# Kernel tuning notes

Measured on AMD Instinct MI355X. Metric: run time of the kernel, lower is better.

Reference implementation:

```python
import jax, jax.numpy as jnp
import numpy as np

N, D, H, O, E, K = 16384, 512, 512, 64, 8, 2


def _layernorm(x, g, b, eps=1e-5):
    mu = jnp.mean(x, axis=-1, keepdims=True)
    var = jnp.var(x, axis=-1, keepdims=True)
    return (x - mu) * jax.lax.rsqrt(var + eps) * g + b


def _gelu(x):
    return jax.nn.gelu(x, approximate=False)  # torch nn.GELU default (erf)


def setup_inputs() -> dict:
    key = jax.random.key(0)
    ks = jax.random.split(key, 20)
    s = 0.02
    return {
        "x": jax.random.normal(ks[0], (N, D), jnp.float32),
        # gate: Linear(D,H) -> LN(H) -> GELU -> Linear(H,E)
        "g_w1": jax.random.normal(ks[1], (D, H), jnp.float32) * s,
        "g_b1": jnp.zeros((H,), jnp.float32),
        "g_ln_g": jnp.ones((H,), jnp.float32),
        "g_ln_b": jnp.zeros((H,), jnp.float32),
        "g_w2": jax.random.normal(ks[2], (H, E), jnp.float32) * s,
        "g_b2": jnp.zeros((E,), jnp.float32),
        # experts (stacked over E): Linear(D,H)+LN+GELU, Linear(H,H)+LN+GELU, Linear(H,O)
        "e_w1": jax.random.normal(ks[3], (E, D, H), jnp.float32) * s,
        "e_b1": jnp.zeros((E, H), jnp.float32),
        "e_ln1_g": jnp.ones((E, H), jnp.float32),
        "e_ln1_b": jnp.zeros((E, H), jnp.float32),
        "e_w2": jax.random.normal(ks[4], (E, H, H), jnp.float32) * s,
        "e_b2": jnp.zeros((E, H), jnp.float32),
        "e_ln2_g": jnp.ones((E, H), jnp.float32),
        "e_ln2_b": jnp.zeros((E, H), jnp.float32),
        "e_w3": jax.random.normal(ks[5], (E, H, O), jnp.float32) * s,
        "e_b3": jnp.zeros((E, O), jnp.float32),
        # output projection Linear(O,O)
        "p_w": jax.random.normal(ks[6], (O, O), jnp.float32) * s,
        "p_b": jnp.zeros((O,), jnp.float32),
    }


def reference(x, g_w1, g_b1, g_ln_g, g_ln_b, g_w2, g_b2,
              e_w1, e_b1, e_ln1_g, e_ln1_b, e_w2, e_b2, e_ln2_g, e_ln2_b,
              e_w3, e_b3, p_w, p_b):
    n = x.shape[0]
    # --- gate ---
    gh = _gelu(_layernorm(x @ g_w1 + g_b1, g_ln_g, g_ln_b))
    gate_logits = gh @ g_w2 + g_b2                      # [N, E]
    gate_weights = jax.nn.softmax(gate_logits, axis=-1)
    top_k_weights, top_k_indices = jax.lax.top_k(gate_weights, K)
    top_k_weights = top_k_weights / jnp.sum(top_k_weights, axis=-1, keepdims=True)
    # dense per-token expert weights [N, E] (sum of top-k weights routed to each expert)
    w_dense = jnp.zeros((n, e_w1.shape[0]), x.dtype).at[
        jnp.arange(n)[:, None], top_k_indices].add(top_k_weights)
    # --- all experts on all tokens (faithful to dense loop) ---
    h1 = _gelu(_layernorm(jnp.einsum('nd,edh->enh', x, e_w1) + e_b1[:, None, :],
                          e_ln1_g[:, None, :], e_ln1_b[:, None, :]))
    h2 = _gelu(_layernorm(jnp.einsum('enh,ehk->enk', h1, e_w2) + e_b2[:, None, :],
                          e_ln2_g[:, None, :], e_ln2_b[:, None, :]))
    expert_out = jnp.einsum('enh,eho->eno', h2, e_w3) + e_b3[:, None, :]  # [E, N, O]
    combined = jnp.einsum('ne,eno->no', w_dense, expert_out)              # [N, O]
    output = combined @ p_w + p_b
    expert_usage = jnp.mean(gate_weights, axis=0)
    return (output, gate_weights, top_k_indices, top_k_weights, expert_usage)
```

## Files before the change

### kernel.cpp

```cpp
#include <hip/hip_runtime.h>
#include <hip/hip_bf16.h>

#define N_TOK 16384
#define MAX_SLOTS 34080
#define MAX_BLOCKS 216

typedef __attribute__((ext_vector_type(8))) short bf16x8;
typedef __attribute__((ext_vector_type(4))) float f32x4;
typedef unsigned short u16;

__device__ __forceinline__ u16 f2bf(float f) {
  __hip_bfloat16 h = __float2bfloat16(f);
  union { __hip_bfloat16 b; u16 u; } c; c.b = h; return c.u;
}
__device__ __forceinline__ float bfbits2f(u16 u) {
  return __uint_as_float(((unsigned)u) << 16);
}
__device__ __forceinline__ float gelu_erf(float x) {
  return 0.5f * x * (1.0f + erff(x * 0.70710678118654752f));
}
__device__ __forceinline__ float gelu_fast(float x) {
  float u = x * (0.79788456f + 0.035677408f * x * x);
  float ex;
  asm("v_exp_f32 %0, %1" : "=v"(ex) : "v"(-2.8853901f * u));
  float den = 1.0f + ex;
  float r;
  asm("v_rcp_f32 %0, %1" : "=v"(r) : "v"(den));
  return x * r;
}
__device__ __forceinline__ void gload16(const u16* g, char* lds) {
  __builtin_amdgcn_global_load_lds(
      (const __attribute__((address_space(1))) void*)g,
      (__attribute__((address_space(3))) void*)lds, 16, 0, 0);
}

__global__ __launch_bounds__(256) void prep_x(const float* __restrict__ x,
                                              u16* __restrict__ xbf,
                                              u16* __restrict__ xlo) {
  size_t i = (size_t)blockIdx.x * 256 + threadIdx.x;
  float4 v = ((const float4*)x)[i];
  float a[4] = {v.x, v.y, v.z, v.w};
  union { u16 us[4]; unsigned long long ll; } hb, lb;
#pragma unroll
  for (int j = 0; j < 4; ++j) {
    u16 hu = f2bf(a[j]);
    hb.us[j] = hu;
    lb.us[j] = f2bf(a[j] - bfbits2f(hu));
  }
  *(unsigned long long*)(xbf + i * 4) = hb.ll;
  *(unsigned long long*)(xlo + i * 4) = lb.ll;
}

template <int C>
__global__ __launch_bounds__(256) void pack_w(const float* __restrict__ src,
                                              u16* __restrict__ dst, int R) {
  __shared__ float tl[64][65];
  const int e = blockIdx.z;
  const int k0 = blockIdx.x * 64, n0 = blockIdx.y * 64;
  const float* s = src + (size_t)e * R * C;
  const int tr = threadIdx.x >> 2;
  const int tc4 = (threadIdx.x & 3) * 16;
#pragma unroll
  for (int j = 0; j < 4; ++j) {
    float4 v = *(const float4*)(s + (size_t)(k0 + tr) * C + n0 + tc4 + j * 4);
    tl[tr][tc4 + j * 4 + 0] = v.x;
    tl[tr][tc4 + j * 4 + 1] = v.y;
    tl[tr][tc4 + j * 4 + 2] = v.z;
    tl[tr][tc4 + j * 4 + 3] = v.w;
  }
  __syncthreads();
  const int nl = threadIdx.x >> 2;
  const int kl = (threadIdx.x & 3) * 16;
  const int n = n0 + nl;
  const int sx = (n >> 1) & 3;
  const int t = (k0 + kl) >> 5;
  const int q0 = ((k0 + kl) & 31) >> 3;
#pragma unroll
  for (int c = 0; c < 2; ++c) {
    int q = q0 + c;
    int p = q ^ sx;
    union { u16 us[8]; unsigned long long ll[2]; } o;
#pragma unroll
    for (int j = 0; j < 8; ++j) o.us[j] = f2bf(tl[kl + c * 8 + j][nl]);
    u16* d = dst + (((size_t)e * (R / 32) + t) * C + n) * 32 + p * 8;
    ((unsigned long long*)d)[0] = o.ll[0];
    ((unsigned long long*)d)[1] = o.ll[1];
  }
}

__global__ __launch_bounds__(256) void prep_wcat(const float* __restrict__ gw1,
                                                 u16* __restrict__ wp) {
  int idx = blockIdx.x * 256 + threadIdx.x;
  int p = idx & 3;
  int n = (idx >> 2) & 511;
  int t = idx >> 11;
  int q = p ^ ((n >> 1) & 3);
  int k0 = t * 32 + q * 8;
  union { u16 us[8]; unsigned long long ll[2]; } o;
#pragma unroll
  for (int j = 0; j < 8; ++j) {
    int k = k0 + j;
    u16 v;
    if (k < 512) {
      v = f2bf(gw1[k * 512 + n]);
    } else if (k < 1024) {
      float w = gw1[(k - 512) * 512 + n];
      v = f2bf(w - bfbits2f(f2bf(w)));
    } else {
      v = f2bf(gw1[(k - 1024) * 512 + n]);
    }
    o.us[j] = v;
  }
  unsigned long long* d = (unsigned long long*)(wp + (size_t)idx * 8);
  d[0] = o.ll[0];
  d[1] = o.ll[1];
}

__global__ __launch_bounds__(256) void prep_w2t(const float* __restrict__ gw2,
                                                float* __restrict__ w2t) {
  int i = blockIdx.x * 256 + threadIdx.x;
  int e = i >> 9, k = i & 511;
  w2t[i] = gw2[k * 8 + e];
}

template <int FM, int ROUTED, int GATHER, int LNOUT, int FAST>
__global__ __launch_bounds__(512, 2) void gemm_core(
    const u16* __restrict__ A, const u16* __restrict__ A2,
    const u16* __restrict__ Wp, long w_estride, int klen, long osplit,
    const float* __restrict__ bias, int b_estride,
    const float* __restrict__ lng, const float* __restrict__ lnb,
    u16* __restrict__ outb, float* __restrict__ outf,
    const int* __restrict__ slot_token, const int* __restrict__ blk_e,
    const int* __restrict__ blk_tok0) {
  constexpr int BM = FM * 32;
  constexpr int AG = FM * 2;
  constexpr int ABYTES = BM * 64;
  constexpr int BUF = ABYTES + 32768;
  constexpr int NL = AG + 32;
  constexpr int L = (NL + 7) / 8;
  constexpr int TSU = 16384;
  extern __shared__ char smem[];

  const int tid = threadIdx.x;
  const int lane = tid & 63;
  const int wv = tid >> 6;
  const int wm = (wv & 1) * (FM * 16);
  const int wn = (wv >> 1) * 128;
  const int l15 = lane & 15;
  const int lk = lane >> 4;
  const int swzk16 = (lk ^ ((l15 >> 1) & 3)) << 4;

  int e, row0, kt0, kbase;
  if (ROUTED) {
    e = blk_e[blockIdx.x];
    if (e < 0) return;
    row0 = blk_tok0[blockIdx.x];
    kt0 = 0; kbase = 0;
  } else {
    e = 0;
    row0 = blockIdx.x * BM;
    kbase = blockIdx.y * klen;
    kt0 = kbase >> 5;
  }
  const u16* We = Wp + (size_t)e * w_estride;

  const int lrq = lane >> 2;
  const int cse = (((lane & 3) ^ ((lane >> 3) & 3)) << 3);
  size_t off[L];
  int ldsoff[L], typ[L];
#pragma unroll
  for (int i = 0; i < L; ++i) {
    int id = wv + 8 * i;
    if (id >= NL) { typ[i] = 2; off[i] = 0; ldsoff[i] = 0; continue; }
    if (id < AG) {
      int lr = id * 16 + lrq;
      long grow = GATHER ? (long)slot_token[row0 + lr] : (long)(row0 + lr);
      off[i] = (size_t)grow * 512 + cse;
      ldsoff[i] = id * 1024 + lane * 16;
      typ[i] = 0;
    } else {
      int bg = id - AG;
      off[i] = (size_t)bg * 512 + lane * 8;
      ldsoff[i] = ABYTES + bg * 1024 + lane * 16;
      typ[i] = 1;
    }
  }

  auto STAGE = [&](int t, char* b) {
    const int kg = kbase + t * 32;
    const u16* Aseg = A;
    int kc = kg;
    if (A2) {
      if (kg >= 1024) { Aseg = A2; kc = kg - 1024; }
      else if (kg >= 512) kc = kg - 512;
    }
    const u16* Bt = We + (size_t)(kt0 + t) * TSU;
#pragma unroll
    for (int i = 0; i < L; ++i) {
      if (typ[i] == 0)      gload16(Aseg + off[i] + kc, b + ldsoff[i]);
      else if (typ[i] == 1) gload16(Bt + off[i], b + ldsoff[i]);
    }
  };

  f32x4 acc[FM][8];
#pragma unroll
  for (int i = 0; i < FM; ++i)
#pragma unroll
    for (int j = 0; j < 8; ++j) acc[i][j] = (f32x4){0.f, 0.f, 0.f, 0.f};

  const int nt = klen / 32;
  char* buf0 = smem;
  char* buf1 = smem + BUF;

  STAGE(0, buf0);
  __syncthreads();
  for (int t = 0; t < nt; ++t) {
    char* cur = (t & 1) ? buf1 : buf0;
    char* nxt = (t & 1) ? buf0 : buf1;
    if (t + 1 < nt) STAGE(t + 1, nxt);
    char* cB = cur + ABYTES;
    bf16x8 af[FM];
#pragma unroll
    for (int fm = 0; fm < FM; ++fm)
      af[fm] = *(const bf16x8*)(cur + (wm + fm * 16 + l15) * 64 + swzk16);
#pragma unroll
    for (int fn = 0; fn < 8; ++fn) {
      bf16x8 bv = *(const bf16x8*)(cB + (wn + fn * 16 + l15) * 64 + swzk16);
#pragma unroll
      for (int fm = 0; fm < FM; ++fm)
        acc[fm][fn] = __builtin_amdgcn_mfma_f32_16x16x32_bf16(
            af[fm], bv, acc[fm][fn], 0, 0, 0);
    }
    __syncthreads();
  }

  if constexpr (LNOUT) {
    const float* be = bias + (size_t)e * b_estride;
    const float* ge = lng + (size_t)e * b_estride;
    const float* bbe = lnb + (size_t)e * b_estride;
    float bias_v[8], g_v[8], b_v[8];
#pragma unroll
    for (int fn = 0; fn < 8; ++fn) {
      int col = wn + fn * 16 + l15;
      bias_v[fn] = be[col]; g_v[fn] = ge[col]; b_v[fn] = bbe[col];
    }
#pragma unroll
    for (int fm = 0; fm < FM; ++fm)
#pragma unroll
      for (int fn = 0; fn < 8; ++fn)
#pragma unroll
        for (int r = 0; r < 4; ++r) acc[fm][fn][r] += bias_v[fn];

    float* redS1 = (float*)smem;
    float* redS2 = redS1 + 4 * BM;
    const int g = wv >> 1;
#pragma unroll
    for (int fm = 0; fm < FM; ++fm)
#pragma unroll
      for (int r = 0; r < 4; ++r) {
        float a1 = 0.f, a2 = 0.f;
#pragma unroll
        for (int fn = 0; fn < 8; ++fn) {
          float v = acc[fm][fn][r];
          a1 += v; a2 += v * v;
        }
#pragma unroll
        for (int m = 1; m < 16; m <<= 1) {
          a1 += __shfl_xor(a1, m, 64);
          a2 += __shfl_xor(a2, m, 64);
        }
        if (l15 == 0) {
          int row = wm + fm * 16 + lk * 4 + r;
          redS1[g * BM + row] = a1;
          redS2[g * BM + row] = a2;
        }
      }
    __syncthreads();
#pragma unroll
    for (int fm = 0; fm < FM; ++fm)
#pragma unroll
      for (int r = 0; r < 4; ++r) {
        int row = wm + fm * 16 + lk * 4 + r;
        float S1 = 0.f, S2 = 0.f;
#pragma unroll
        for (int q = 0; q < 4; ++q) {
          S1 += redS1[q * BM + row];
          S2 += redS2[q * BM + row];
        }
        float mu = S1 * (1.0f / 512.0f);
        float var = S2 * (1.0f / 512.0f) - mu * mu;
        float rs = rsqrtf(var + 1e-5f);
        size_t rowg = (size_t)(row0 + row);
#pragma unroll
        for (int fn = 0; fn < 8; ++fn) {
          int col = wn + fn * 16 + l15;
          float v = (acc[fm][fn][r] - mu) * rs * g_v[fn] + b_v[fn];
          v = FAST ? gelu_fast(v) : gelu_erf(v);
          outb[rowg * 512 + col] = f2bf(v);
        }
      }
  } else {
    float* dst = outf + (size_t)blockIdx.y * osplit;
#pragma unroll
    for (int fm = 0; fm < FM; ++fm)
#pragma unroll
      for (int r = 0; r < 4; ++r) {
        size_t rowg = (size_t)(row0 + wm + fm * 16 + lk * 4 + r);
#pragma unroll
        for (int fn = 0; fn < 8; ++fn)
          dst[rowg * 512 + wn + fn * 16 + l15] = acc[fm][fn][r];
      }
  }
}

__global__ __launch_bounds__(256) void gate2_topk(
    const float* __restrict__ gh0, const float* __restrict__ gh1,
    const float* __restrict__ b1, const float* __restrict__ lng,
    const float* __restrict__ lnb, const float* __restrict__ w2t,
    const float* __restrict__ b2, float* __restrict__ gwout,
    float* __restrict__ idxout, float* __restrict__ tkwout) {
  const int lane = threadIdx.x & 63;
  const int wv = threadIdx.x >> 6;
  const int t = blockIdx.x * 4 + wv;
  const int c0 = lane * 8;
  float v[8];
  {
    float4 a0 = *(const float4*)(gh0 + (size_t)t * 512 + c0);
    float4 a1 = *(const float4*)(gh0 + (size_t)t * 512 + c0 + 4);
    float4 h0 = *(const float4*)(gh1 + (size_t)t * 512 + c0);
    float4 h1 = *(const float4*)(gh1 + (size_t)t * 512 + c0 + 4);
    float4 bb0 = *(const float4*)(b1 + c0);
    float4 bb1 = *(const float4*)(b1 + c0 + 4);
    v[0] = a0.x + h0.x + bb0.x; v[1] = a0.y + h0.y + bb0.y;
    v[2] = a0.z + h0.z + bb0.z; v[3] = a0.w + h0.w + bb0.w;
    v[4] = a1.x + h1.x + bb1.x; v[5] = a1.y + h1.y + bb1.y;
    v[6] = a1.z + h1.z + bb1.z; v[7] = a1.w + h1.w + bb1.w;
  }
  float s1 = 0.f, s2 = 0.f;
#pragma unroll
  for (int j = 0; j < 8; ++j) { s1 += v[j]; s2 += v[j] * v[j]; }
#pragma unroll
  for (int m = 1; m < 64; m <<= 1) {
    s1 += __shfl_xor(s1, m, 64);
    s2 += __shfl_xor(s2, m, 64);
  }
  float mu = s1 * (1.0f / 512.0f);
  float var = s2 * (1.0f / 512.0f) - mu * mu;
  float rs = rsqrtf(var + 1e-5f);
  float y[8];
  {
    float4 g0 = *(const float4*)(lng + c0);
    float4 g1 = *(const float4*)(lng + c0 + 4);
    float4 q0 = *(const float4*)(lnb + c0);
    float4 q1 = *(const float4*)(lnb + c0 + 4);
    float gg[8] = {g0.x, g0.y, g0.z, g0.w, g1.x, g1.y, g1.z, g1.w};
    float qq[8] = {q0.x, q0.y, q0.z, q0.w, q1.x, q1.y, q1.z, q1.w};
#pragma unroll
    for (int j = 0; j < 8; ++j)
      y[j] = gelu_erf((v[j] - mu) * rs * gg[j] + qq[j]);
  }
  float logit[8];
#pragma unroll
  for (int e = 0; e < 8; ++e) {
    const float4* wr = (const float4*)(w2t + e * 512 + c0);
    float4 w0 = wr[0], w1 = wr[1];
    float p = y[0] * w0.x + y[1] * w0.y + y[2] * w0.z + y[3] * w0.w +
              y[4] * w1.x + y[5] * w1.y + y[6] * w1.z + y[7] * w1.w;
#pragma unroll
    for (int m = 1; m < 64; m <<= 1) p += __shfl_xor(p, m, 64);
    logit[e] = p + b2[e];
  }
  if (lane == 0) {
    float mx = logit[0];
#pragma unroll
    for (int e = 1; e < 8; ++e) mx = fmaxf(mx, logit[e]);
    float w[8], ssum = 0.f;
#pragma unroll
    for (int e = 0; e < 8; ++e) { w[e] = expf(logit[e] - mx); ssum += w[e]; }
    float inv = 1.0f / ssum;
#pragma unroll
    for (int e = 0; e < 8; ++e) w[e] *= inv;
    float w1v = -1.f, w2v = -1.f; int i1 = 0, i2 = 0;
#pragma unroll
    for (int e = 0; e < 8; ++e) {
      float vv = w[e];
      if (vv > w1v)      { w2v = w1v; i2 = i1; w1v = vv; i1 = e; }
      else if (vv > w2v) { w2v = vv; i2 = e; }
    }
    float s = w1v + w2v;
#pragma unroll
    for (int e = 0; e < 8; ++e) gwout[t * 8 + e] = w[e];
    idxout[t * 2] = (float)i1; idxout[t * 2 + 1] = (float)i2;
    tkwout[t * 2] = w1v / s;   tkwout[t * 2 + 1] = w2v / s;
  }
}

__global__ __launch_bounds__(256) void usage_k(const float* __restrict__ gw,
                                               float* __restrict__ usage) {
  __shared__ float r[256];
  int e = blockIdx.x;
  float s = 0.f;
  for (int t = threadIdx.x; t < N_TOK; t += 256) s += gw[t * 8 + e];
  r[threadIdx.x] = s;
  __syncthreads();
  for (int st = 128; st > 0; st >>= 1) {
    if (threadIdx.x < st) r[threadIdx.x] += r[threadIdx.x + st];
    __syncthreads();
  }
  if (threadIdx.x == 0) usage[e] = r[0] * (1.0f / (float)N_TOK);
}

__global__ __launch_bounds__(256) void count_hist(const float* __restrict__ idxout,
                                                  int* __restrict__ blk_cnt) {
  __shared__ int h[8];
  if (threadIdx.x < 8) h[threadIdx.x] = 0;
  __syncthreads();
  int t = blockIdx.x * 256 + threadIdx.x;
  int e0 = (int)idxout[t * 2], e1 = (int)idxout[t * 2 + 1];
  atomicAdd(&h[e0], 1);
  atomicAdd(&h[e1], 1);
  __syncthreads();
  if (threadIdx.x < 8) blk_cnt[blockIdx.x * 8 + threadIdx.x] = h[threadIdx.x];
}

__global__ __launch_bounds__(512) void k_offsets2(
    const int* __restrict__ blk_cnt, int* __restrict__ sbase,
    int* __restrict__ blk_e, int* __restrict__ blk_tok0) {
  __shared__ int cnt[64][8];
  __shared__ int ecnt[8];
  __shared__ int offs[8];
  const int tid = threadIdx.x;
  cnt[tid >> 3][tid & 7] = blk_cnt[tid];
  __syncthreads();
  if (tid < 8) {
    int s = 0;
    for (int b = 0; b < 64; ++b) s += cnt[b][tid];
    ecnt[tid] = s;
  }
  __syncthreads();
  if (tid == 0) {
    int off = 0;
    for (int e = 0; e < 8; ++e) {
      offs[e] = off;
      off += ((ecnt[e] + 159) / 160) * 160;
    }
  }
  __syncthreads();
  {
    int b = tid >> 3, e = tid & 7;
    int s = offs[e];
    for (int bp = 0; bp < b; ++bp) s += cnt[bp][e];
    sbase[tid] = s;
  }
  for (int b = tid; b < MAX_BLOCKS; b += 512) {
    int acc = 0, be = -1, bt = 0;
#pragma unroll
    for (int e = 0; e < 8; ++e) {
      int nbe = (ecnt[e] + 159) / 160;
      if (b >= acc && b < acc + nbe) { be = e; bt = offs[e] + (b - acc) * 160; }
      acc += nbe;
    }
    blk_e[b] = be;
    blk_tok0[b] = bt;
  }
}

__global__ __launch_bounds__(256) void k_padinit(int* __restrict__ slot_token,
                                                 float* __restrict__ slot_w) {
  int i = blockIdx.x * 256 + threadIdx.x;
  if (i < MAX_SLOTS) { slot_token[i] = 0; slot_w[i] = 0.f; }
}

__global__ __launch_bounds__(256) void k_scatter2(
    const float* __restrict__ idxout, const float* __restrict__ tkwout,
    const int* __restrict__ sbase, int* __restrict__ slot_token,
    float* __restrict__ slot_w, int* __restrict__ tok_slot) {
  __shared__ int lpos[8];
  if (threadIdx.x < 8) lpos[threadIdx.x] = 0;
  __syncthreads();
  int t = blockIdx.x * 256 + threadIdx.x;
#pragma unroll
  for (int k = 0; k < 2; ++k) {
    int e = (int)idxout[t * 2 + k];
    int lr = atomicAdd(&lpos[e], 1);
    int s = sbase[blockIdx.x * 8 + e] + lr;
    slot_token[s] = t;
    slot_w[s] = tkwout[t * 2 + k];
    tok_slot[t * 2 + k] = s;
  }
}

__global__ __launch_bounds__(512) void gemm3_eo(
    const u16* __restrict__ h, const u16* __restrict__ w3p,
    const float* __restrict__ b3, const float* __restrict__ slot_w,
    const int* __restrict__ blk_e, const int* __restrict__ blk_tok0,
    float* __restrict__ eo) {
  constexpr int ABYTES = 10240;
  constexpr int BUF = ABYTES + 4096;
  __shared__ char smem[2][BUF];
  int e = blk_e[blockIdx.x];
  if (e < 0) return;
  int row0 = blk_tok0[blockIdx.x];

  const int tid = threadIdx.x;
  const int lane = tid & 63;
  const int wv = tid >> 6;
  const int wm = (wv & 1) * 80;
  const int wn = (wv >> 1) * 16;
  const int l15 = lane & 15, lk = lane >> 4;
  const int swzk16 = (lk ^ ((l15 >> 1) & 3)) << 4;
  const u16* we = w3p + (size_t)e * 32768;

  const int lrq = lane >> 2;
  const int cse = (((lane & 3) ^ ((lane >> 3) & 3)) << 3);
  size_t off[2];
  int ldsoff[2], typ[2];
#pragma unroll
  for (int i = 0; i < 2; ++i) {
    int id = wv + 8 * i;
    if (id >= 14) { typ[i] = 2; off[i] = 0; ldsoff[i] = 0; continue; }
    if (id < 10) {
      off[i] = (size_t)(row0 + id * 16 + lrq) * 512 + cse;
      ldsoff[i] = id * 1024 + lane * 16;
      typ[i] = 0;
    } else {
      int bg = id - 10;
      off[i] = (size_t)bg * 512 + lane * 8;
      ldsoff[i] = ABYTES + bg * 1024 + lane * 16;
      typ[i] = 1;
    }
  }

  auto STAGE = [&](int t, char* b) {
#pragma unroll
    for (int i = 0; i < 2; ++i) {
      if (typ[i] == 0)      gload16(h + off[i] + t * 32, b + ldsoff[i]);
      else if (typ[i] == 1) gload16(we + (size_t)t * 2048 + off[i], b + ldsoff[i]);
    }
  };

  f32x4 acc[5];
#pragma unroll
  for (int j = 0; j < 5; ++j) acc[j] = (f32x4){0.f, 0.f, 0.f, 0.f};

  STAGE(0, smem[0]);
  __syncthreads();
  for (int t = 0; t < 16; ++t) {
    char* cur = smem[t & 1];
    if (t + 1 < 16) STAGE(t + 1, smem[(t + 1) & 1]);
    char* cB = cur + ABYTES;
    bf16x8 bv = *(const bf16x8*)(cB + (wn + l15) * 64 + swzk16);
#pragma unroll
    for (int fm = 0; fm < 5; ++fm) {
      bf16x8 a = *(const bf16x8*)(cur + (wm + fm * 16 + l15) * 64 + swzk16);
      acc[fm] = __builtin_amdgcn_mfma_f32_16x16x32_bf16(a, bv, acc[fm], 0, 0, 0);
    }
    __syncthreads();
  }

#pragma unroll
  for (int fm = 0; fm < 5; ++fm)
#pragma unroll
    for (int r = 0; r < 4; ++r) {
      int row = wm + fm * 16 + lk * 4 + r;
      float w = slot_w[row0 + row];
      int col = wn + l15;
      eo[(size_t)(row0 + row) * 64 + col] = w * (acc[fm][r] + b3[e * 64 + col]);
    }
}

__global__ __launch_bounds__(256) void combine_proj(
    const float* __restrict__ eo, const int* __restrict__ tok_slot,
    const float* __restrict__ pw, const float* __restrict__ pb,
    float* __restrict__ outp) {
  __shared__ float cs[64][68];
  __shared__ float pws[64][68];
  const int t0 = blockIdx.x * 64;
  const int tq = threadIdx.x & 3;
  const int tt = threadIdx.x >> 2;
#pragma unroll
  for (int j = 0; j < 4; ++j) {
    float4 v = *(const float4*)(pw + tt * 64 + tq * 16 + j * 4);
    *(float4*)&pws[tt][tq * 16 + j * 4] = v;
  }
  {
    int t = t0 + tt;
    int s1 = tok_slot[t * 2], s2 = tok_slot[t * 2 + 1];
#pragma unroll
    for (int j = 0; j < 4; ++j) {
      float4 a = *(const float4*)(eo + (size_t)s1 * 64 + tq * 16 + j * 4);
      float4 b = *(const float4*)(eo + (size_t)s2 * 64 + tq * 16 + j * 4);
      float4 c = {a.x + b.x, a.y + b.y, a.z + b.z, a.w + b.w};
      *(float4*)&cs[tt][tq * 16 + j * 4] = c;
    }
  }
  __syncthreads();
  float o[16];
#pragma unroll
  for (int i = 0; i < 16; ++i) o[i] = 0.f;
  for (int j = 0; j < 64; ++j) {
    float c = cs[tt][j];
#pragma unroll
    for (int q4 = 0; q4 < 4; ++q4) {
      float4 p = *(const float4*)&pws[j][tq * 16 + q4 * 4];
      o[q4 * 4 + 0] += c * p.x;
      o[q4 * 4 + 1] += c * p.y;
      o[q4 * 4 + 2] += c * p.z;
      o[q4 * 4 + 3] += c * p.w;
    }
  }
#pragma unroll
  for (int i = 0; i < 16; ++i)
    outp[(size_t)(t0 + tt) * 64 + tq * 16 + i] = o[i] + pb[tq * 16 + i];
}

extern "C" void kernel_launch(void* const* d_in, const int* in_sizes, int n_in,
                              void* d_out, int out_size, void* d_ws, size_t ws_size,
                              hipStream_t stream) {
  const float* x      = (const float*)d_in[0];
  const float* g_w1   = (const float*)d_in[1];
  const float* g_b1   = (const float*)d_in[2];
  const float* g_lng  = (const float*)d_in[3];
  const float* g_lnb  = (const float*)d_in[4];
  const float* g_w2   = (const float*)d_in[5];
  const float* g_b2   = (const float*)d_in[6];
  const float* e_w1   = (const float*)d_in[7];
  const float* e_b1   = (const float*)d_in[8];
  const float* e_ln1g = (const float*)d_in[9];
  const float* e_ln1b = (const float*)d_in[10];
  const float* e_w2   = (const float*)d_in[11];
  const float* e_b2   = (const float*)d_in[12];
  const float* e_ln2g = (const float*)d_in[13];
  const float* e_ln2b = (const float*)d_in[14];
  const float* e_w3   = (const float*)d_in[15];
  const float* e_b3   = (const float*)d_in[16];
  const float* p_w    = (const float*)d_in[17];
  const float* p_b    = (const float*)d_in[18];

  char* ws = (char*)d_ws;
  u16*   x_bf  = (u16*)(ws);
  u16*   x_lo  = (u16*)(ws + (16ull << 20));
  u16*   e_w1p = (u16*)(ws + (32ull << 20));
  u16*   e_w2p = (u16*)(ws + (36ull << 20));
  u16*   e_w3p = (u16*)(ws + (40ull << 20));
  u16*   wcat  = (u16*)(ws + (41ull << 20));
  float* w2t   = (float*)(ws + (43ull << 20));
  float* gh0   = (float*)(ws + (44ull << 20));
  float* gh1   = (float*)(ws + (76ull << 20));
  u16*   h     = (u16*)(ws + (44ull << 20));
  float* eo    = (float*)(ws + (112ull << 20));
  int*   slot_token = (int*)(ws + (121ull << 20));
  float* slot_w     = (float*)(ws + (121ull << 20) + (1ull << 18));
  int*   tok_slot   = (int*)(ws + (121ull << 20) + (2ull << 18));
  int*   blk_cnt    = (int*)(ws + (122ull << 20));
  int*   sbase      = blk_cnt + 512;
  int*   blk_e      = blk_cnt + 1024;
  int*   blk_tok0   = blk_cnt + 2048;
  if (ws_size < (123ull << 20)) return;

  float* fout = (float*)d_out;
  float* o_output = fout;
  float* o_gatew  = fout + 1048576;
  float* o_idx    = fout + 1179648;
  float* o_topw   = fout + 1212416;
  float* o_usage  = fout + 1245184;

  (void)hipFuncSetAttribute((const void*)gemm_core<4, 0, 0, 0, 0>,
                            hipFuncAttributeMaxDynamicSharedMemorySize, 81920);
  (void)hipFuncSetAttribute((const void*)gemm_core<5, 1, 1, 1, 1>,
                            hipFuncAttributeMaxDynamicSharedMemorySize, 86016);
  (void)hipFuncSetAttribute((const void*)gemm_core<5, 1, 0, 1, 1>,
                            hipFuncAttributeMaxDynamicSharedMemorySize, 86016);

  prep_x<<<8192, 256, 0, stream>>>(x, x_bf, x_lo);
  pack_w<512><<<dim3(8, 8, 8), 256, 0, stream>>>(e_w1, e_w1p, 512);
  pack_w<512><<<dim3(8, 8, 8), 256, 0, stream>>>(e_w2, e_w2p, 512);
  pack_w<64><<<dim3(8, 1, 8), 256, 0, stream>>>(e_w3, e_w3p, 512);
  prep_wcat<<<384, 256, 0, stream>>>(g_w1, wcat);
  prep_w2t<<<16, 256, 0, stream>>>(g_w2, w2t);

  gemm_core<4, 0, 0, 0, 0><<<dim3(N_TOK / 128, 2), 512, 81920, stream>>>(
      x_bf, x_lo, wcat, 0, 768, (long)N_TOK * 512, nullptr, 0,
      nullptr, nullptr, nullptr, gh0, nullptr, nullptr, nullptr);
  gate2_topk<<<N_TOK / 4, 256, 0, stream>>>(gh0, gh1, g_b1, g_lng, g_lnb,
                                            w2t, g_b2, o_gatew, o_idx, o_topw);
  usage_k<<<8, 256, 0, stream>>>(o_gatew, o_usage);

  count_hist<<<64, 256, 0, stream>>>(o_idx, blk_cnt);
  k_offsets2<<<1, 512, 0, stream>>>(blk_cnt, sbase, blk_e, blk_tok0);
  k_padinit<<<(MAX_SLOTS + 255) / 256, 256, 0, stream>>>(slot_token, slot_w);
  k_scatter2<<<64, 256, 0, stream>>>(o_idx, o_topw, sbase, slot_token, slot_w,
                                     tok_slot);

  gemm_core<5, 1, 1, 1, 1><<<MAX_BLOCKS, 512, 86016, stream>>>(
      x_bf, nullptr, e_w1p, 512 * 512, 512, 0, e_b1, 512,
      e_ln1g, e_ln1b, h, nullptr, slot_token, blk_e, blk_tok0);
  gemm_core<5, 1, 0, 1, 1><<<MAX_BLOCKS, 512, 86016, stream>>>(
      h, nullptr, e_w2p, 512 * 512, 512, 0, e_b2, 512,
      e_ln2g, e_ln2b, h, nullptr, slot_token, blk_e, blk_tok0);
  gemm3_eo<<<MAX_BLOCKS, 512, 0, stream>>>(h, e_w3p, e_b3, slot_w, blk_e,
                                           blk_tok0, eo);
  combine_proj<<<N_TOK / 64, 256, 0, stream>>>(eo, tok_slot, p_w, p_b, o_output);
}
```

Before: 208.5 us.

## Triple-buffer GEMM LDS staging with explicit vmcnt waits and split barriers

```diff
diff --git a/kernel.cpp b/kernel.cpp
--- a/kernel.cpp
+++ b/kernel.cpp
@@ -8,6 +8,9 @@
 typedef __attribute__((ext_vector_type(8))) short bf16x8;
 typedef __attribute__((ext_vector_type(4))) float f32x4;
 typedef unsigned short u16;
+
+#define V_WAIT(N) asm volatile("s_waitcnt vmcnt(" #N ")" ::: "memory")
+#define LGKM0()   asm volatile("s_waitcnt lgkmcnt(0)" ::: "memory")
 
 __device__ __forceinline__ u16 f2bf(float f) {
   __hip_bfloat16 h = __float2bfloat16(f);
@@ -186,6 +189,18 @@
     }
   }
 
+  float bias_v[8], g_v[8], b_v[8];
+  if constexpr (LNOUT) {
+    const float* be = bias + (size_t)e * b_estride;
+    const float* ge = lng + (size_t)e * b_estride;
+    const float* bbe = lnb + (size_t)e * b_estride;
+#pragma unroll
+    for (int fn = 0; fn < 8; ++fn) {
+      int col = wn + fn * 16 + l15;
+      bias_v[fn] = be[col]; g_v[fn] = ge[col]; b_v[fn] = bbe[col];
+    }
+  }
+
   auto STAGE = [&](int t, char* b) {
     const int kg = kbase + t * 32;
     const u16* Aseg = A;
@@ -209,15 +224,25 @@
     for (int j = 0; j < 8; ++j) acc[i][j] = (f32x4){0.f, 0.f, 0.f, 0.f};
 
   const int nt = klen / 32;
-  char* buf0 = smem;
-  char* buf1 = smem + BUF;
-
-  STAGE(0, buf0);
-  __syncthreads();
+
+  V_WAIT(0);
+  STAGE(0, smem);
+  STAGE(1, smem + BUF);
+  STAGE(2, smem + 2 * BUF);
+
+  int bsel = 0;
   for (int t = 0; t < nt; ++t) {
-    char* cur = (t & 1) ? buf1 : buf0;
-    char* nxt = (t & 1) ? buf0 : buf1;
-    if (t + 1 < nt) STAGE(t + 1, nxt);
+    if constexpr (FM == 5) {
+      if (t < nt - 2)       { if (wv < 2) V_WAIT(12); else V_WAIT(10); }
+      else if (t == nt - 2) { if (wv < 2) V_WAIT(6);  else V_WAIT(5); }
+      else                  V_WAIT(0);
+    } else {
+      if (t < nt - 2)       V_WAIT(10);
+      else if (t == nt - 2) V_WAIT(5);
+      else                  V_WAIT(0);
+    }
+    __builtin_amdgcn_s_barrier();
+    char* cur = smem + bsel * BUF;
     char* cB = cur + ABYTES;
     bf16x8 af[FM];
 #pragma unroll
@@ -231,19 +256,13 @@
         acc[fm][fn] = __builtin_amdgcn_mfma_f32_16x16x32_bf16(
             af[fm], bv, acc[fm][fn], 0, 0, 0);
     }
-    __syncthreads();
+    LGKM0();
+    __builtin_amdgcn_s_barrier();
+    if (t + 3 < nt) STAGE(t + 3, cur);
+    bsel = (bsel == 2) ? 0 : bsel + 1;
   }
 
   if constexpr (LNOUT) {
-    const float* be = bias + (size_t)e * b_estride;
-    const float* ge = lng + (size_t)e * b_estride;
-    const float* bbe = lnb + (size_t)e * b_estride;
-    float bias_v[8], g_v[8], b_v[8];
-#pragma unroll
-    for (int fn = 0; fn < 8; ++fn) {
-      int col = wn + fn * 16 + l15;
-      bias_v[fn] = be[col]; g_v[fn] = ge[col]; b_v[fn] = bbe[col];
-    }
 #pragma unroll
     for (int fm = 0; fm < FM; ++fm)
 #pragma unroll
@@ -497,7 +516,7 @@
     float* __restrict__ eo) {
   constexpr int ABYTES = 10240;
   constexpr int BUF = ABYTES + 4096;
-  __shared__ char smem[2][BUF];
+  __shared__ char smem[3 * BUF];
   int e = blk_e[blockIdx.x];
   if (e < 0) return;
   int row0 = blk_tok0[blockIdx.x];
@@ -531,6 +550,19 @@
     }
   }
 
+  float b3v = b3[e * 64 + wn + l15];
+  float swv[5];
+#pragma unroll
+  for (int fm = 0; fm < 5; ++fm)
+    swv[fm] = slot_w[row0 + wm + fm * 16 + lk * 4];
+  float swr[5][4];
+#pragma unroll
+  for (int fm = 0; fm < 5; ++fm)
+#pragma unroll
+    for (int r = 0; r < 4; ++r)
+      swr[fm][r] = slot_w[row0 + wm + fm * 16 + lk * 4 + r];
+  (void)swv;
+
   auto STAGE = [&](int t, char* b) {
 #pragma unroll
     for (int i = 0; i < 2; ++i) {
@@ -543,11 +575,18 @@
 #pragma unroll
   for (int j = 0; j < 5; ++j) acc[j] = (f32x4){0.f, 0.f, 0.f, 0.f};
 
-  STAGE(0, smem[0]);
-  __syncthreads();
+  V_WAIT(0);
+  STAGE(0, smem);
+  STAGE(1, smem + BUF);
+  STAGE(2, smem + 2 * BUF);
+
+  int bsel = 0;
   for (int t = 0; t < 16; ++t) {
-    char* cur = smem[t & 1];
-    if (t + 1 < 16) STAGE(t + 1, smem[(t + 1) & 1]);
+    if (t < 14)       { if (wv < 6) V_WAIT(4); else V_WAIT(2); }
+    else if (t == 14) { if (wv < 6) V_WAIT(2); else V_WAIT(1); }
+    else              V_WAIT(0);
+    __builtin_amdgcn_s_barrier();
+    char* cur = smem + bsel * BUF;
     char* cB = cur + ABYTES;
     bf16x8 bv = *(const bf16x8*)(cB + (wn + l15) * 64 + swzk16);
 #pragma unroll
@@ -555,7 +594,10 @@
       bf16x8 a = *(const bf16x8*)(cur + (wm + fm * 16 + l15) * 64 + swzk16);
       acc[fm] = __builtin_amdgcn_mfma_f32_16x16x32_bf16(a, bv, acc[fm], 0, 0, 0);
     }
-    __syncthreads();
+    LGKM0();
+    __builtin_amdgcn_s_barrier();
+    if (t + 3 < 16) STAGE(t + 3, cur);
+    bsel = (bsel == 2) ? 0 : bsel + 1;
   }
 
 #pragma unroll
@@ -563,9 +605,7 @@
 #pragma unroll
     for (int r = 0; r < 4; ++r) {
       int row = wm + fm * 16 + lk * 4 + r;
-      float w = slot_w[row0 + row];
-      int col = wn + l15;
-      eo[(size_t)(row0 + row) * 64 + col] = w * (acc[fm][r] + b3[e * 64 + col]);
+      eo[(size_t)(row0 + row) * 64 + wn + l15] = swr[fm][r] * (acc[fm][r] + b3v);
     }
 }
 
@@ -666,11 +706,11 @@
   float* o_usage  = fout + 1245184;
 
   (void)hipFuncSetAttribute((const void*)gemm_core<4, 0, 0, 0, 0>,
-                            hipFuncAttributeMaxDynamicSharedMemorySize, 81920);
+                            hipFuncAttributeMaxDynamicSharedMemorySize, 122880);
   (void)hipFuncSetAttribute((const void*)gemm_core<5, 1, 1, 1, 1>,
-                            hipFuncAttributeMaxDynamicSharedMemorySize, 86016);
+                            hipFuncAttributeMaxDynamicSharedMemorySize, 129024);
   (void)hipFuncSetAttribute((const void*)gemm_core<5, 1, 0, 1, 1>,
-                            hipFuncAttributeMaxDynamicSharedMemorySize, 86016);
+                            hipFuncAttributeMaxDynamicSharedMemorySize, 129024);
 
   prep_x<<<8192, 256, 0, stream>>>(x, x_bf, x_lo);
   pack_w<512><<<dim3(8, 8, 8), 256, 0, stream>>>(e_w1, e_w1p, 512);
@@ -679,7 +719,7 @@
   prep_wcat<<<384, 256, 0, stream>>>(g_w1, wcat);
   prep_w2t<<<16, 256, 0, stream>>>(g_w2, w2t);
 
-  gemm_core<4, 0, 0, 0, 0><<<dim3(N_TOK / 128, 2), 512, 81920, stream>>>(
+  gemm_core<4, 0, 0, 0, 0><<<dim3(N_TOK / 128, 2), 512, 122880, stream>>>(
       x_bf, x_lo, wcat, 0, 768, (long)N_TOK * 512, nullptr, 0,
       nullptr, nullptr, nullptr, gh0, nullptr, nullptr, nullptr);
   gate2_topk<<<N_TOK / 4, 256, 0, stream>>>(gh0, gh1, g_b1, g_lng, g_lnb,
@@ -692,10 +732,10 @@
   k_scatter2<<<64, 256, 0, stream>>>(o_idx, o_topw, sbase, slot_token, slot_w,
                                      tok_slot);
 
-  gemm_core<5, 1, 1, 1, 1><<<MAX_BLOCKS, 512, 86016, stream>>>(
+  gemm_core<5, 1, 1, 1, 1><<<MAX_BLOCKS, 512, 129024, stream>>>(
       x_bf, nullptr, e_w1p, 512 * 512, 512, 0, e_b1, 512,
       e_ln1g, e_ln1b, h, nullptr, slot_token, blk_e, blk_tok0);
-  gemm_core<5, 1, 0, 1, 1><<<MAX_BLOCKS, 512, 86016, stream>>>(
+  gemm_core<5, 1, 0, 1, 1><<<MAX_BLOCKS, 512, 129024, stream>>>(
       h, nullptr, e_w2p, 512 * 512, 512, 0, e_b2, 512,
       e_ln2g, e_ln2b, h, nullptr, slot_token, blk_e, blk_tok0);
   gemm3_eo<<<MAX_BLOCKS, 512, 0, stream>>>(h, e_w3p, e_b3, slot_w, blk_e,
```

Measured after the change: 212.5 us. No clear change (+1.9%).
